# Performance work log

Measured on AMD Instinct MI355X. Metric: run time of the kernel, lower is better.

Reference implementation:

```python
import jax, jax.numpy as jnp
import numpy as np

N_DEG = 5
RANK = 4
SCALE = 4
IMW = IMH = 512
S = IMW * IMH
BATCH = 64
C_CH = 1


def setup_inputs() -> dict:
    key = jax.random.key(0)
    k1, k2, k3, k4 = jax.random.split(key, 4)
    x = jax.random.normal(k1, (BATCH, C_CH, IMW // SCALE, IMH // SCALE), dtype=jnp.float32)
    # CP-decomposed polynomial (CCP) factors; small init keeps degree-5 products stable
    A = jax.random.normal(k2, (N_DEG, RANK, S), dtype=jnp.float32) * 0.01
    C = jax.random.normal(k3, (S, RANK), dtype=jnp.float32) * 0.01
    b = jax.random.normal(k4, (S,), dtype=jnp.float32) * 0.01
    return {"x": x, "A": A, "C": C, "b": b}


def reference(x, A, C, b):
    bsize, c, w, h = x.shape
    # bilinear upsample, align_corners=False (half-pixel, matches torch default)
    up = jax.image.resize(x, (bsize, c, w * SCALE, h * SCALE), method="bilinear")
    flat = up.reshape(bsize, c, S)
    v = flat[:, c - 1, :]  # [B, S] -- original applies PolyLayer only to channel c-1
    # CCP polynomial network: z1 = A1 v; z_n = (A_n v) * z_{n-1} + z_{n-1}
    za = jnp.einsum("nrs,bs->bnr", A, v)  # [B, N, rank]
    z = za[:, 0]
    for n in range(1, N_DEG):
        z = za[:, n] * z + z
    out_v = jnp.einsum("br,sr->bs", z, C) + b  # [B, S]
    flat = flat.at[:, c - 1, :].set(out_v)
    return flat.reshape(bsize, c, w * SCALE, h * SCALE)
```

## Files before the change

kernel.cpp:

```cpp
#include <hip/hip_runtime.h>

#define S_TOTAL (512 * 512)
#define BATCH 64
#define KTOT2 16384
#define NKC 64

typedef float vfloat4 __attribute__((ext_vector_type(4)));

__device__ __forceinline__ float swz_x1(float v) {
    return __int_as_float(__builtin_amdgcn_ds_swizzle(__float_as_int(v), 0x041F));
}
__device__ __forceinline__ float swz_x2(float v) {
    return __int_as_float(__builtin_amdgcn_ds_swizzle(__float_as_int(v), 0x081F));
}
__device__ __forceinline__ float swz_x4(float v) {
    return __int_as_float(__builtin_amdgcn_ds_swizzle(__float_as_int(v), 0x101F));
}
__device__ __forceinline__ float swz_x8(float v) {
    return __int_as_float(__builtin_amdgcn_ds_swizzle(__float_as_int(v), 0x201F));
}

__global__ __launch_bounds__(256) void adjxy_kernel(
    const float* __restrict__ A,
    float* __restrict__ B2)
{
    __shared__ float b1loc[20][128];

    const int t  = threadIdx.x;
    const int nr = blockIdx.x >> 5;
    const int tc = blockIdx.x & 31;
    const int y0 = 16 * tc - 2;

    const float* An = A + (size_t)nr * S_TOTAL;

#pragma unroll
    for (int i = t; i < 20 * 128; i += 256) {
        const int rl = i >> 7;
        const int j  = i & 127;
        const int y  = y0 + rl;
        float s = 0.0f;
        if (y >= 0 && y < 512) {
            const float* Ay = An + (size_t)y * 512;
            const int base = 4 * j;
            const vfloat4 m0 = *(const vfloat4*)(Ay + max(base - 4, 0));
            const vfloat4 m1 = *(const vfloat4*)(Ay + base);
            const vfloat4 m2 = *(const vfloat4*)(Ay + min(base + 4, 508));
            float e0 = m0.z, e1 = m0.w, e6 = m2.x, e7 = m2.y;
            if (j == 0)   { e0 = 0.0f; e1 = 0.0f; }
            if (j == 127) { e6 = 0.0f; e7 = 0.0f; }
            s = 0.125f * e0 + 0.375f * e1
              + 0.625f * m1.x + 0.875f * m1.y
              + 0.875f * m1.z + 0.625f * m1.w
              + 0.375f * e6 + 0.125f * e7;
            if (j == 0)   s += 0.375f * Ay[0]   + 0.125f * Ay[1];
            if (j == 127) s += 0.125f * Ay[510] + 0.375f * Ay[511];
        }
        b1loc[rl][j] = s;
    }
    __syncthreads();

    const float w[8] = {0.125f, 0.375f, 0.625f, 0.875f,
                        0.875f, 0.625f, 0.375f, 0.125f};
#pragma unroll
    for (int i = t; i < 512; i += 256) {
        const int tyl = i >> 7;
        const int j   = i & 127;
        const int ty  = tc * 4 + tyl;
        float s = 0.0f;
#pragma unroll
        for (int p = 0; p < 8; ++p)
            s = fmaf(w[p], b1loc[4 * tyl + p][j], s);
        if (ty == 0)   s += 0.375f * b1loc[2][j]  + 0.125f * b1loc[3][j];
        if (ty == 127) s += 0.125f * b1loc[16][j] + 0.375f * b1loc[17][j];
        B2[(size_t)nr * KTOT2 + ty * 128 + j] = s;
    }
}

__global__ __launch_bounds__(512) void za_partial_kernel(
    const float* __restrict__ x,
    const float* __restrict__ B2,
    float* __restrict__ partial)
{
    const int t    = threadIdx.x;
    const int kc   = blockIdx.x >> 2;
    const int bq   = blockIdx.x & 3;
    const int wv   = t >> 6;
    const int lane = t & 63;
    const int b0   = bq * 16 + wv * 2;
    const size_t kbase = (size_t)kc * 256 + 4 * lane;

    vfloat4 xv0 = *(const vfloat4*)(x + (size_t)b0 * KTOT2 + kbase);
    vfloat4 xv1 = *(const vfloat4*)(x + (size_t)(b0 + 1) * KTOT2 + kbase);

    float* pb = partial + (size_t)kc * 1280;
    const int lane1 = lane & 1, lane2 = lane & 2;

#pragma unroll
    for (int ch = 0; ch < 2; ++ch) {
        float acc[4][5];
#pragma unroll
        for (int v = 0; v < 4; ++v)
#pragma unroll
            for (int tt = 0; tt < 5; ++tt) acc[v][tt] = 0.0f;

#pragma unroll
        for (int tt = 0; tt < 5; ++tt)
#pragma unroll
            for (int par = 0; par < 2; ++par) {
                const int nr = ch * 10 + 2 * tt + par;
                const vfloat4 bq4 = *(const vfloat4*)(B2 + (size_t)nr * KTOT2 + kbase);
                acc[par][tt] =
                    fmaf(bq4.x, xv0.x, fmaf(bq4.y, xv0.y,
                    fmaf(bq4.z, xv0.z, fmaf(bq4.w, xv0.w, acc[par][tt]))));
                acc[2 + par][tt] =
                    fmaf(bq4.x, xv1.x, fmaf(bq4.y, xv1.y,
                    fmaf(bq4.z, xv1.z, fmaf(bq4.w, xv1.w, acc[2 + par][tt]))));
            }

        float s1[2][5];
#pragma unroll
        for (int v = 0; v < 2; ++v)
#pragma unroll
            for (int tt = 0; tt < 5; ++tt) {
                const float u = acc[v][tt], h = acc[v + 2][tt];
                s1[v][tt] = (lane1 ? h : u) + swz_x1(lane1 ? u : h);
            }
        float s2[5];
#pragma unroll
        for (int tt = 0; tt < 5; ++tt) {
            const float u = s1[0][tt], h = s1[1][tt];
            s2[tt] = (lane2 ? h : u) + swz_x2(lane2 ? u : h);
        }
#pragma unroll
        for (int tt = 0; tt < 5; ++tt) {
            s2[tt] += swz_x4(s2[tt]);
            s2[tt] += swz_x8(s2[tt]);
            s2[tt] += __shfl_xor(s2[tt], 16, 64);
            s2[tt] += __shfl_xor(s2[tt], 32, 64);
        }

        if (lane < 4) {
            const int bi  = lane & 1;
            const int par = (lane >> 1) & 1;
            float* dst = pb + (size_t)(b0 + bi) * 20 + ch * 10 + par;
#pragma unroll
            for (int tt = 0; tt < 5; ++tt) dst[2 * tt] = s2[tt];
        }
    }
}

__global__ __launch_bounds__(256) void za_reduce_kernel(
    const float* __restrict__ partial, float* __restrict__ za)
{
    const int c = blockIdx.x * 256 + threadIdx.x;
    float a0 = 0, a1 = 0, a2 = 0, a3 = 0;
    for (int r = 0; r < NKC; r += 4) {
        a0 += partial[(size_t)(r + 0) * 1280 + c];
        a1 += partial[(size_t)(r + 1) * 1280 + c];
        a2 += partial[(size_t)(r + 2) * 1280 + c];
        a3 += partial[(size_t)(r + 3) * 1280 + c];
    }
    za[c] = (a0 + a1) + (a2 + a3);
}

__global__ __launch_bounds__(256) void out_kernel(
    const float* __restrict__ C,
    const float* __restrict__ bias,
    const float* __restrict__ za,
    float* __restrict__ out)
{
    __shared__ float zs[256];
    const int t = threadIdx.x;
    if (t < 64) {
#pragma unroll
        for (int r = 0; r < 4; ++r) {
            float zv = za[t * 20 + r];
#pragma unroll
            for (int n = 1; n < 5; ++n)
                zv *= (1.0f + za[t * 20 + n * 4 + r]);
            zs[t * 4 + r] = zv;
        }
    }
    __syncthreads();

    const int sb = blockIdx.x >> 1;
    const int bh = blockIdx.x & 1;
    const int s0 = (sb * 256 + t) * 4;
    const vfloat4 c0 = *(const vfloat4*)(C + (size_t)s0 * 4);
    const vfloat4 c1 = *(const vfloat4*)(C + (size_t)s0 * 4 + 4);
    const vfloat4 c2 = *(const vfloat4*)(C + (size_t)s0 * 4 + 8);
    const vfloat4 c3 = *(const vfloat4*)(C + (size_t)s0 * 4 + 12);
    const vfloat4 bv = *(const vfloat4*)(bias + s0);

#pragma unroll 8
    for (int bb = bh * 32; bb < bh * 32 + 32; ++bb) {
        const float z0 = zs[bb * 4 + 0], z1 = zs[bb * 4 + 1];
        const float z2 = zs[bb * 4 + 2], z3 = zs[bb * 4 + 3];
        vfloat4 o;
        o.x = fmaf(z0, c0.x, fmaf(z1, c0.y, fmaf(z2, c0.z, fmaf(z3, c0.w, bv.x))));
        o.y = fmaf(z0, c1.x, fmaf(z1, c1.y, fmaf(z2, c1.z, fmaf(z3, c1.w, bv.y))));
        o.z = fmaf(z0, c2.x, fmaf(z1, c2.y, fmaf(z2, c2.z, fmaf(z3, c2.w, bv.z))));
        o.w = fmaf(z0, c3.x, fmaf(z1, c3.y, fmaf(z2, c3.z, fmaf(z3, c3.w, bv.w))));
        __builtin_nontemporal_store(o, (vfloat4*)(out + (size_t)bb * S_TOTAL + s0));
    }
}

extern "C" void kernel_launch(void* const* d_in, const int* in_sizes, int n_in,
                              void* d_out, int out_size, void* d_ws, size_t ws_size,
                              hipStream_t stream)
{
    const float* x    = (const float*)d_in[0];
    const float* A    = (const float*)d_in[1];
    const float* C    = (const float*)d_in[2];
    const float* bias = (const float*)d_in[3];
    float* out = (float*)d_out;

    float* B2      = (float*)d_ws;
    float* partial = B2 + (size_t)20 * KTOT2;
    float* za      = partial + (size_t)NKC * 1280;

    adjxy_kernel<<<640, 256, 0, stream>>>(A, B2);
    za_partial_kernel<<<256, 512, 0, stream>>>(x, B2, partial);
    za_reduce_kernel<<<5, 256, 0, stream>>>(partial, za);
    out_kernel<<<512, 256, 0, stream>>>(C, bias, za, out);
}
```

Measured before the change: 34.93 us.

## Fold za reduction into partial and output kernels, drop reduce launch

The za_partial kernel now gives each block four k-chunks across its waves and reduces them in shared memory, producing 16 partial rows instead of 64. The separate za_reduce kernel is removed. Each out_kernel block sums the 16 partials itself before computing the polynomial. This saves one kernel launch and its serialization gap, at the cost of every output block redundantly reading 16x1280 partials.

```diff
diff --git a/kernel.cpp b/kernel.cpp
--- a/kernel.cpp
+++ b/kernel.cpp
@@ -3,7 +3,7 @@
 #define S_TOTAL (512 * 512)
 #define BATCH 64
 #define KTOT2 16384
-#define NKC 64
+#define NPR 16
 
 typedef float vfloat4 __attribute__((ext_vector_type(4)));
 
@@ -81,18 +81,22 @@
     const float* __restrict__ B2,
     float* __restrict__ partial)
 {
+    __shared__ float red[4][80];
+
     const int t    = threadIdx.x;
-    const int kc   = blockIdx.x >> 2;
-    const int bq   = blockIdx.x & 3;
+    const int kc4  = blockIdx.x >> 4;
+    const int bqn  = blockIdx.x & 15;
     const int wv   = t >> 6;
     const int lane = t & 63;
-    const int b0   = bq * 16 + wv * 2;
+    const int kcl  = wv & 3;
+    const int bh   = wv >> 2;
+    const int kc   = kc4 * 4 + kcl;
+    const int b0   = bqn * 4 + bh * 2;
     const size_t kbase = (size_t)kc * 256 + 4 * lane;
 
-    vfloat4 xv0 = *(const vfloat4*)(x + (size_t)b0 * KTOT2 + kbase);
-    vfloat4 xv1 = *(const vfloat4*)(x + (size_t)(b0 + 1) * KTOT2 + kbase);
-
-    float* pb = partial + (size_t)kc * 1280;
+    const vfloat4 xv0 = *(const vfloat4*)(x + (size_t)b0 * KTOT2 + kbase);
+    const vfloat4 xv1 = *(const vfloat4*)(x + (size_t)(b0 + 1) * KTOT2 + kbase);
+
     const int lane1 = lane & 1, lane2 = lane & 2;
 
 #pragma unroll
@@ -142,46 +146,30 @@
         if (lane < 4) {
             const int bi  = lane & 1;
             const int par = (lane >> 1) & 1;
-            float* dst = pb + (size_t)(b0 + bi) * 20 + ch * 10 + par;
-#pragma unroll
-            for (int tt = 0; tt < 5; ++tt) dst[2 * tt] = s2[tt];
-        }
-    }
-}
-
-__global__ __launch_bounds__(256) void za_reduce_kernel(
-    const float* __restrict__ partial, float* __restrict__ za)
-{
-    const int c = blockIdx.x * 256 + threadIdx.x;
-    float a0 = 0, a1 = 0, a2 = 0, a3 = 0;
-    for (int r = 0; r < NKC; r += 4) {
-        a0 += partial[(size_t)(r + 0) * 1280 + c];
-        a1 += partial[(size_t)(r + 1) * 1280 + c];
-        a2 += partial[(size_t)(r + 2) * 1280 + c];
-        a3 += partial[(size_t)(r + 3) * 1280 + c];
-    }
-    za[c] = (a0 + a1) + (a2 + a3);
+#pragma unroll
+            for (int tt = 0; tt < 5; ++tt)
+                red[kcl][(bh * 2 + bi) * 20 + ch * 10 + 2 * tt + par] = s2[tt];
+        }
+    }
+
+    __syncthreads();
+    if (t < 80) {
+        const float s = red[0][t] + red[1][t] + red[2][t] + red[3][t];
+        const int bl = t / 20;
+        const int nr = t - bl * 20;
+        partial[(size_t)kc4 * 1280 + (bqn * 4 + bl) * 20 + nr] = s;
+    }
 }
 
 __global__ __launch_bounds__(256) void out_kernel(
     const float* __restrict__ C,
     const float* __restrict__ bias,
-    const float* __restrict__ za,
+    const float* __restrict__ partial,
     float* __restrict__ out)
 {
+    __shared__ float za_sh[1280];
     __shared__ float zs[256];
     const int t = threadIdx.x;
-    if (t < 64) {
-#pragma unroll
-        for (int r = 0; r < 4; ++r) {
-            float zv = za[t * 20 + r];
-#pragma unroll
-            for (int n = 1; n < 5; ++n)
-                zv *= (1.0f + za[t * 20 + n * 4 + r]);
-            zs[t * 4 + r] = zv;
-        }
-    }
-    __syncthreads();
 
     const int sb = blockIdx.x >> 1;
     const int bh = blockIdx.x & 1;
@@ -191,6 +179,32 @@
     const vfloat4 c2 = *(const vfloat4*)(C + (size_t)s0 * 4 + 8);
     const vfloat4 c3 = *(const vfloat4*)(C + (size_t)s0 * 4 + 12);
     const vfloat4 bv = *(const vfloat4*)(bias + s0);
+
+#pragma unroll
+    for (int q = 0; q < 5; ++q) {
+        const int c = q * 256 + t;
+        float a0 = 0, a1 = 0, a2 = 0, a3 = 0;
+#pragma unroll
+        for (int r = 0; r < NPR; r += 4) {
+            a0 += partial[(size_t)(r + 0) * 1280 + c];
+            a1 += partial[(size_t)(r + 1) * 1280 + c];
+            a2 += partial[(size_t)(r + 2) * 1280 + c];
+            a3 += partial[(size_t)(r + 3) * 1280 + c];
+        }
+        za_sh[c] = (a0 + a1) + (a2 + a3);
+    }
+    __syncthreads();
+    if (t < 64) {
+#pragma unroll
+        for (int r = 0; r < 4; ++r) {
+            float zv = za_sh[t * 20 + r];
+#pragma unroll
+            for (int n = 1; n < 5; ++n)
+                zv *= (1.0f + za_sh[t * 20 + n * 4 + r]);
+            zs[t * 4 + r] = zv;
+        }
+    }
+    __syncthreads();
 
 #pragma unroll 8
     for (int bb = bh * 32; bb < bh * 32 + 32; ++bb) {
@@ -217,10 +231,8 @@
 
     float* B2      = (float*)d_ws;
     float* partial = B2 + (size_t)20 * KTOT2;
-    float* za      = partial + (size_t)NKC * 1280;
 
     adjxy_kernel<<<640, 256, 0, stream>>>(A, B2);
     za_partial_kernel<<<256, 512, 0, stream>>>(x, B2, partial);
-    za_reduce_kernel<<<5, 256, 0, stream>>>(partial, za);
-    out_kernel<<<512, 256, 0, stream>>>(C, bias, za, out);
-}
+    out_kernel<<<512, 256, 0, stream>>>(C, bias, partial, out);
+}
```

Result: faster. 33.27 us (-4.8%).
